# Kernel optimization log

Measured on AMD Instinct MI355X. Metric: run time of the kernel, lower is better.

Reference implementation:

```python
import jax, jax.numpy as jnp
import numpy as np

S = 14        # grid size
B = 2         # boxes per cell
NC = 20       # classes
N = 4096      # batch
L_COORD = 5.0
L_NOOBJ = 0.5


def _xywh2xyxy(b):
    # b[..., :2] are cell-center coords (scaled by 1/S), b[..., 2:4] are w,h
    xy = b[..., :2] / S
    wh = b[..., 2:4]
    return jnp.concatenate([xy - 0.5 * wh, xy + 0.5 * wh], axis=-1)


def _iou(b1, b2):
    # elementwise (broadcasting) IoU over last dim [x1,y1,x2,y2]
    lt = jnp.maximum(b1[..., :2], b2[..., :2])
    rb = jnp.minimum(b1[..., 2:4], b2[..., 2:4])
    wh = jnp.clip(rb - lt, 0.0)
    inter = wh[..., 0] * wh[..., 1]
    a1 = (b1[..., 2] - b1[..., 0]) * (b1[..., 3] - b1[..., 1])
    a2 = (b2[..., 2] - b2[..., 0]) * (b2[..., 3] - b2[..., 1])
    return inter / (a1 + a2 - inter)


def setup_inputs() -> dict:
    key = jax.random.key(0)
    k1, k2, k3, k4 = jax.random.split(key, 4)
    pred_tensor = jax.random.uniform(k1, (N, S, S, B * 5 + NC), dtype=jnp.float32)
    target_boxes = jax.random.uniform(k2, (N, S, S, 4), dtype=jnp.float32)
    target_cls = jax.random.uniform(k3, (N, S, S, NC), dtype=jnp.float32)
    has_object_map = jax.random.bernoulli(k4, 0.15, (N, S, S))
    return dict(pred_tensor=pred_tensor, target_boxes=target_boxes,
                target_cls=target_cls, has_object_map=has_object_map)


def reference(pred_tensor, target_boxes, target_cls, has_object_map):
    n = pred_tensor.shape[0]
    pb = pred_tensor[..., :B * 5].reshape(n, S, S, B, 5)   # (N,S,S,B,5)
    pcls = pred_tensor[..., B * 5:]                        # (N,S,S,20)
    m = has_object_map                                     # (N,S,S) bool
    mf = m.astype(pred_tensor.dtype)

    # class loss: masked sum of squares over object cells
    cls_loss = jnp.sum(jnp.where(m[..., None], (pcls - target_cls) ** 2, 0.0))

    # no-object loss: confidence^2 summed over non-object cells, both boxes
    noobj_loss = jnp.sum(jnp.where(~m[..., None], pb[..., 4] ** 2, 0.0))

    # best-iou box selection (iou is treated as ground truth: no gradient)
    iou = _iou(_xywh2xyxy(pb[..., :4]),
               _xywh2xyxy(target_boxes)[..., None, :])    # (N,S,S,B)
    iou = jax.lax.stop_gradient(iou)
    best = jnp.argmax(iou, axis=-1)                        # (N,S,S)
    best_iou = jnp.max(iou, axis=-1)                       # (N,S,S)
    resp = jnp.take_along_axis(pb, best[..., None, None], axis=3)[..., 0, :]  # (N,S,S,5)

    reg_loss = (jnp.sum(mf[..., None] * (resp[..., :2] - target_boxes[..., :2]) ** 2)
                + jnp.sum(mf[..., None] * (jnp.sqrt(resp[..., 2:4])
                                           - jnp.sqrt(target_boxes[..., 2:4])) ** 2))

    # containing-object confidence loss vs best iou (target detached)
    contain_loss = jnp.sum(mf * (resp[..., 4] - best_iou) ** 2)

    total = (L_COORD * reg_loss + L_NOOBJ * noobj_loss + contain_loss + cls_loss) / n
    return jnp.stack([total, reg_loss, contain_loss, noobj_loss, cls_loss])
```

## Files before the change

### kernel.cpp

```cpp
#include <hip/hip_runtime.h>


#define GS 14
#define NCLS 20
#define BLOCK 256
#define CPT 2
#define CPB (BLOCK * CPT)
#define NSLOTS 64
#define SLOT_STRIDE 16


template <int CB>
__device__ __forceinline__ void cell_compute(const float (&v)[60],
                                             const float4 tb4,
                                             const float* __restrict__ tcls,
                                             int cell, bool m,
                                             float& reg, float& cont,
                                             float& noobj, float& cls) {
    const float invS = 1.0f / (float)GS;
    if (m) {
        const float tx = tb4.x, ty = tb4.y, tw = tb4.z, th = tb4.w;

        const float tcx = tx * invS, tcy = ty * invS;
        const float t_x1 = tcx - 0.5f * tw, t_y1 = tcy - 0.5f * th;
        const float t_x2 = tcx + 0.5f * tw, t_y2 = tcy + 0.5f * th;
        const float ta = (t_x2 - t_x1) * (t_y2 - t_y1);

        const float b0x = v[CB + 0], b0y = v[CB + 1], b0w = v[CB + 2], b0h = v[CB + 3], b0c = v[CB + 4];
        const float b1x = v[CB + 5], b1y = v[CB + 6], b1w = v[CB + 7], b1h = v[CB + 8], b1c = v[CB + 9];

        float iou0, iou1;
        {
            const float cx = b0x * invS, cy = b0y * invS;
            const float x1 = cx - 0.5f * b0w, y1 = cy - 0.5f * b0h;
            const float x2 = cx + 0.5f * b0w, y2 = cy + 0.5f * b0h;
            const float iw = fmaxf(fminf(x2, t_x2) - fmaxf(x1, t_x1), 0.0f);
            const float ih = fmaxf(fminf(y2, t_y2) - fmaxf(y1, t_y1), 0.0f);
            const float inter = iw * ih;
            const float pa = (x2 - x1) * (y2 - y1);
            iou0 = inter / (pa + ta - inter);
        }
        {
            const float cx = b1x * invS, cy = b1y * invS;
            const float x1 = cx - 0.5f * b1w, y1 = cy - 0.5f * b1h;
            const float x2 = cx + 0.5f * b1w, y2 = cy + 0.5f * b1h;
            const float iw = fmaxf(fminf(x2, t_x2) - fmaxf(x1, t_x1), 0.0f);
            const float ih = fmaxf(fminf(y2, t_y2) - fmaxf(y1, t_y1), 0.0f);
            const float inter = iw * ih;
            const float pa = (x2 - x1) * (y2 - y1);
            iou1 = inter / (pa + ta - inter);
        }

        const bool sel1 = iou1 > iou0;
        const float biou = fmaxf(iou0, iou1);
        const float rx = sel1 ? b1x : b0x;
        const float ry = sel1 ? b1y : b0y;
        const float rw = sel1 ? b1w : b0w;
        const float rh = sel1 ? b1h : b0h;
        const float rc = sel1 ? b1c : b0c;

        const float d0 = rx - tx, d1 = ry - ty;
        const float d2 = sqrtf(rw) - sqrtf(tw);
        const float d3 = sqrtf(rh) - sqrtf(th);
        reg += d0 * d0 + d1 * d1 + d2 * d2 + d3 * d3;

        const float dc = rc - biou;
        cont += dc * dc;

        const float4* tc4 = reinterpret_cast<const float4*>(tcls + (size_t)cell * NCLS);
        float csum = 0.0f;
        #pragma unroll
        for (int j = 0; j < 5; ++j) {
            const float4 t4 = tc4[j];
            float d;
            d = v[CB + 10 + j * 4 + 0] - t4.x; csum += d * d;
            d = v[CB + 10 + j * 4 + 1] - t4.y; csum += d * d;
            d = v[CB + 10 + j * 4 + 2] - t4.z; csum += d * d;
            d = v[CB + 10 + j * 4 + 3] - t4.w; csum += d * d;
        }
        cls += csum;
    } else {
        const float c0 = v[CB + 4], c1 = v[CB + 9];
        noobj += c0 * c0 + c1 * c1;
    }
}

__launch_bounds__(BLOCK)
__global__ void yolo_loss_kernel(const float* __restrict__ pred,
                                 const float* __restrict__ tbox,
                                 const float* __restrict__ tcls,
                                 const void* __restrict__ mask,
                                 float* __restrict__ ws,
                                 int ncells) {
    const int tid = threadIdx.x;

    int my_gt1 = 0, my_nzoff = 0;
    if (ncells >= 4096) {
        const uint4 w4 = reinterpret_cast<const uint4*>(mask)[tid];
        const unsigned a = w4.x | w4.y | w4.z | w4.w;
        my_gt1   = (a & 0xFEFEFEFEu) != 0;
        my_nzoff = (a & 0xFFFFFF00u) != 0;
    } else if (tid == 0) {
        const unsigned char* mb = (const unsigned char*)mask;
        for (int i = 0; i < ncells; ++i) {
            if (mb[i] > 1) my_gt1 = 1;
            if ((i & 3) != 0 && mb[i] != 0) my_nzoff = 1;
        }
    }
    const int gt1   = __syncthreads_or(my_gt1);
    const int nzoff = __syncthreads_or(my_nzoff);
    const int fmt = gt1 ? 2 : (nzoff ? 1 : 0);

    const int g = blockIdx.x * BLOCK + tid;
    const int c0 = g * CPT;

    float reg = 0.0f, cont = 0.0f, noobj = 0.0f, cls = 0.0f;

    if (c0 + CPT <= ncells) {
        float v[60];
        float4* v4 = reinterpret_cast<float4*>(v);
        const float4* prow = reinterpret_cast<const float4*>(pred) + (size_t)g * 15;
        #pragma unroll
        for (int j = 0; j < 15; ++j) v4[j] = prow[j];

        bool m0, m1;
        if (fmt == 2) {
            const float2 mm = reinterpret_cast<const float2*>(mask)[g];
            m0 = mm.x != 0.0f; m1 = mm.y != 0.0f;
        } else if (fmt == 1) {
            const uchar2 mm = reinterpret_cast<const uchar2*>(mask)[g];
            m0 = mm.x != 0; m1 = mm.y != 0;
        } else {
            const int2 mm = reinterpret_cast<const int2*>(mask)[g];
            m0 = mm.x != 0; m1 = mm.y != 0;
        }

        const float4 tb0 = reinterpret_cast<const float4*>(tbox)[c0];
        const float4 tb1 = reinterpret_cast<const float4*>(tbox)[c0 + 1];

        cell_compute<0>(v, tb0, tcls, c0,     m0, reg, cont, noobj, cls);
        cell_compute<30>(v, tb1, tcls, c0 + 1, m1, reg, cont, noobj, cls);
    } else if (c0 < ncells) {
        for (int cell = c0; cell < ncells; ++cell) {
            bool m;
            if (fmt == 2)      m = ((const float*)mask)[cell] != 0.0f;
            else if (fmt == 1) m = ((const unsigned char*)mask)[cell] != 0;
            else               m = ((const int*)mask)[cell] != 0;
            float v[60];
            #pragma unroll
            for (int f = 0; f < 30; ++f) v[f] = pred[(size_t)cell * 30 + f];
            float4 tb;
            tb.x = tbox[(size_t)cell * 4 + 0];
            tb.y = tbox[(size_t)cell * 4 + 1];
            tb.z = tbox[(size_t)cell * 4 + 2];
            tb.w = tbox[(size_t)cell * 4 + 3];
            cell_compute<0>(v, tb, tcls, cell, m, reg, cont, noobj, cls);
        }
    }

    #pragma unroll
    for (int off = 32; off > 0; off >>= 1) {
        reg   += __shfl_down(reg, off);
        cont  += __shfl_down(cont, off);
        noobj += __shfl_down(noobj, off);
        cls   += __shfl_down(cls, off);
    }

    __shared__ float sred[4][4];
    const int wave = tid >> 6;
    if ((tid & 63) == 0) {
        sred[wave][0] = reg; sred[wave][1] = cont;
        sred[wave][2] = noobj; sred[wave][3] = cls;
    }
    __syncthreads();
    if (tid == 0) {
        float r = 0, c = 0, no = 0, cl = 0;
        #pragma unroll
        for (int w = 0; w < 4; ++w) {
            r += sred[w][0]; c += sred[w][1]; no += sred[w][2]; cl += sred[w][3];
        }
        float* slot = ws + (size_t)(blockIdx.x & (NSLOTS - 1)) * SLOT_STRIDE;
        atomicAdd(&slot[0], r);
        atomicAdd(&slot[1], c);
        atomicAdd(&slot[2], no);
        atomicAdd(&slot[3], cl);
    }
}

__global__ void yolo_finalize_kernel(const float* __restrict__ ws,
                                     float* __restrict__ out, float inv_n) {
    const int t = threadIdx.x;
    float reg   = ws[t * SLOT_STRIDE + 0];
    float cont  = ws[t * SLOT_STRIDE + 1];
    float noobj = ws[t * SLOT_STRIDE + 2];
    float cls   = ws[t * SLOT_STRIDE + 3];
    #pragma unroll
    for (int off = 32; off > 0; off >>= 1) {
        reg   += __shfl_down(reg, off);
        cont  += __shfl_down(cont, off);
        noobj += __shfl_down(noobj, off);
        cls   += __shfl_down(cls, off);
    }
    if (t == 0) {
        const float total = (5.0f * reg + 0.5f * noobj + cont + cls) * inv_n;
        out[0] = total;
        out[1] = reg;
        out[2] = cont;
        out[3] = noobj;
        out[4] = cls;
    }
}

extern "C" void kernel_launch(void* const* d_in, const int* in_sizes, int n_in,
                              void* d_out, int out_size, void* d_ws, size_t ws_size,
                              hipStream_t stream) {
    const float* pred = (const float*)d_in[0];
    const float* tbox = (const float*)d_in[1];
    const float* tcls = (const float*)d_in[2];
    const void*  mask = d_in[3];
    float* ws  = (float*)d_ws;
    float* out = (float*)d_out;

    const int ncells = in_sizes[3];
    const int n_img  = ncells / (GS * GS);
    const float inv_n = 1.0f / (float)n_img;

    hipMemsetAsync(ws, 0, NSLOTS * SLOT_STRIDE * sizeof(float), stream);

    const int grid = (ncells + CPB - 1) / CPB;
    yolo_loss_kernel<<<grid, BLOCK, 0, stream>>>(pred, tbox, tcls, mask, ws, ncells);

    yolo_finalize_kernel<<<1, 64, 0, stream>>>(ws, out, inv_n);
}
```

Before: 34.95 us.

## Skip unneeded pred loads for empty cell pairs and fuse finalize via last-block reduction

Loads only the float4s holding the confidence values for both cells up front, and fetches the rest of the prediction row only when at least one of the two cells has an object. This cuts HBM traffic for the roughly 72% of pairs with no object. It also removes the separate finalize kernel: each block writes its partials to its own slot, and the last block to arrive (found with an atomic counter) reduces all slots and writes the output. The counter reset is folded into a smaller memset. The cost is a threadfence plus atomic per block, and the last block reduces serially over about 1568 slots.

```diff
diff --git a/kernel.cpp b/kernel.cpp
--- a/kernel.cpp
+++ b/kernel.cpp
@@ -6,9 +6,8 @@
 #define BLOCK 256
 #define CPT 2
 #define CPB (BLOCK * CPT)
-#define NSLOTS 64
-#define SLOT_STRIDE 16
-
+
+#define WS_SLOT0 16
 
 template <int CB>
 __device__ __forceinline__ void cell_compute(const float (&v)[60],
@@ -91,25 +90,25 @@
                                  const float* __restrict__ tcls,
                                  const void* __restrict__ mask,
                                  float* __restrict__ ws,
-                                 int ncells) {
+                                 int ncells, float inv_n,
+                                 float* __restrict__ out) {
     const int tid = threadIdx.x;
 
-    int my_gt1 = 0, my_nzoff = 0;
+    int my_bits = 0;
     if (ncells >= 4096) {
         const uint4 w4 = reinterpret_cast<const uint4*>(mask)[tid];
         const unsigned a = w4.x | w4.y | w4.z | w4.w;
-        my_gt1   = (a & 0xFEFEFEFEu) != 0;
-        my_nzoff = (a & 0xFFFFFF00u) != 0;
+        my_bits  = ((a & 0xFEFEFEFEu) != 0) ? 2 : 0;
+        my_bits |= ((a & 0xFFFFFF00u) != 0) ? 1 : 0;
     } else if (tid == 0) {
         const unsigned char* mb = (const unsigned char*)mask;
         for (int i = 0; i < ncells; ++i) {
-            if (mb[i] > 1) my_gt1 = 1;
-            if ((i & 3) != 0 && mb[i] != 0) my_nzoff = 1;
-        }
-    }
-    const int gt1   = __syncthreads_or(my_gt1);
-    const int nzoff = __syncthreads_or(my_nzoff);
-    const int fmt = gt1 ? 2 : (nzoff ? 1 : 0);
+            if (mb[i] > 1) my_bits |= 2;
+            if ((i & 3) != 0 && mb[i] != 0) my_bits |= 1;
+        }
+    }
+    const int bits = __syncthreads_or(my_bits);
+    const int fmt = (bits & 2) ? 2 : ((bits & 1) ? 1 : 0);
 
     const int g = blockIdx.x * BLOCK + tid;
     const int c0 = g * CPT;
@@ -120,8 +119,11 @@
         float v[60];
         float4* v4 = reinterpret_cast<float4*>(v);
         const float4* prow = reinterpret_cast<const float4*>(pred) + (size_t)g * 15;
-        #pragma unroll
-        for (int j = 0; j < 15; ++j) v4[j] = prow[j];
+
+        v4[1] = prow[1];
+        v4[2] = prow[2];
+        v4[8] = prow[8];
+        v4[9] = prow[9];
 
         bool m0, m1;
         if (fmt == 2) {
@@ -137,6 +139,14 @@
 
         const float4 tb0 = reinterpret_cast<const float4*>(tbox)[c0];
         const float4 tb1 = reinterpret_cast<const float4*>(tbox)[c0 + 1];
+
+        if (m0 | m1) {
+            v4[0] = prow[0];
+            v4[3] = prow[3]; v4[4] = prow[4]; v4[5] = prow[5];
+            v4[6] = prow[6]; v4[7] = prow[7];
+            v4[10] = prow[10]; v4[11] = prow[11]; v4[12] = prow[12];
+            v4[13] = prow[13]; v4[14] = prow[14];
+        }
 
         cell_compute<0>(v, tb0, tcls, c0,     m0, reg, cont, noobj, cls);
         cell_compute<30>(v, tb1, tcls, c0 + 1, m1, reg, cont, noobj, cls);
@@ -167,47 +177,58 @@
     }
 
     __shared__ float sred[4][4];
+    __shared__ int s_last;
     const int wave = tid >> 6;
     if ((tid & 63) == 0) {
         sred[wave][0] = reg; sred[wave][1] = cont;
         sred[wave][2] = noobj; sred[wave][3] = cls;
     }
     __syncthreads();
+
     if (tid == 0) {
         float r = 0, c = 0, no = 0, cl = 0;
         #pragma unroll
         for (int w = 0; w < 4; ++w) {
             r += sred[w][0]; c += sred[w][1]; no += sred[w][2]; cl += sred[w][3];
         }
-        float* slot = ws + (size_t)(blockIdx.x & (NSLOTS - 1)) * SLOT_STRIDE;
-        atomicAdd(&slot[0], r);
-        atomicAdd(&slot[1], c);
-        atomicAdd(&slot[2], no);
-        atomicAdd(&slot[3], cl);
-    }
-}
-
-__global__ void yolo_finalize_kernel(const float* __restrict__ ws,
-                                     float* __restrict__ out, float inv_n) {
-    const int t = threadIdx.x;
-    float reg   = ws[t * SLOT_STRIDE + 0];
-    float cont  = ws[t * SLOT_STRIDE + 1];
-    float noobj = ws[t * SLOT_STRIDE + 2];
-    float cls   = ws[t * SLOT_STRIDE + 3];
-    #pragma unroll
-    for (int off = 32; off > 0; off >>= 1) {
-        reg   += __shfl_down(reg, off);
-        cont  += __shfl_down(cont, off);
-        noobj += __shfl_down(noobj, off);
-        cls   += __shfl_down(cls, off);
-    }
-    if (t == 0) {
-        const float total = (5.0f * reg + 0.5f * noobj + cont + cls) * inv_n;
-        out[0] = total;
-        out[1] = reg;
-        out[2] = cont;
-        out[3] = noobj;
-        out[4] = cls;
+        reinterpret_cast<float4*>(ws + WS_SLOT0)[blockIdx.x] = make_float4(r, c, no, cl);
+        __threadfence();
+        const int prev = atomicAdd((int*)ws, 1);
+        s_last = (prev == (int)gridDim.x - 1);
+    }
+    __syncthreads();
+
+    if (s_last) {
+        __threadfence();
+        float r = 0, c = 0, no = 0, cl = 0;
+        for (int b = tid; b < (int)gridDim.x; b += BLOCK) {
+            const float4 p = reinterpret_cast<const float4*>(ws + WS_SLOT0)[b];
+            r += p.x; c += p.y; no += p.z; cl += p.w;
+        }
+        #pragma unroll
+        for (int off = 32; off > 0; off >>= 1) {
+            r  += __shfl_down(r, off);
+            c  += __shfl_down(c, off);
+            no += __shfl_down(no, off);
+            cl += __shfl_down(cl, off);
+        }
+        if ((tid & 63) == 0) {
+            sred[wave][0] = r; sred[wave][1] = c;
+            sred[wave][2] = no; sred[wave][3] = cl;
+        }
+        __syncthreads();
+        if (tid == 0) {
+            float R = 0, C = 0, NO = 0, CL = 0;
+            #pragma unroll
+            for (int w = 0; w < 4; ++w) {
+                R += sred[w][0]; C += sred[w][1]; NO += sred[w][2]; CL += sred[w][3];
+            }
+            out[0] = (5.0f * R + 0.5f * NO + C + CL) * inv_n;
+            out[1] = R;
+            out[2] = C;
+            out[3] = NO;
+            out[4] = CL;
+        }
     }
 }
 
@@ -225,10 +246,9 @@
     const int n_img  = ncells / (GS * GS);
     const float inv_n = 1.0f / (float)n_img;
 
-    hipMemsetAsync(ws, 0, NSLOTS * SLOT_STRIDE * sizeof(float), stream);
+    hipMemsetAsync(ws, 0, sizeof(int), stream);
 
     const int grid = (ncells + CPB - 1) / CPB;
-    yolo_loss_kernel<<<grid, BLOCK, 0, stream>>>(pred, tbox, tcls, mask, ws, ncells);
-
-    yolo_finalize_kernel<<<1, 64, 0, stream>>>(ws, out, inv_n);
+    yolo_loss_kernel<<<grid, BLOCK, 0, stream>>>(pred, tbox, tcls, mask, ws,
+                                                 ncells, inv_n, out);
 }
```

New measurement: 84.61 us. 2.42x slower.

## Split confidence-sum pass from object-cell pass and skip loads for empty cells

Applied to the files above, without the earlier changes.

The kernel now launches two interleaved block roles. One role streams the whole prediction tensor with coalesced float4 loads and sums the squared confidences of all cells. The other role loads prediction rows, target boxes and class targets only for object cells, then subtracts their confidences from the no-object sum. The goal is to cut the memory traffic of the per-cell pass, where about 85% of cells have no object. The catch is that the prediction tensor is still read in full, only ~2/15 of the float4 lines are useful in the streaming pass, and the subtraction can add floating-point cancellation.

```diff
diff --git a/kernel.cpp b/kernel.cpp
--- a/kernel.cpp
+++ b/kernel.cpp
@@ -12,13 +12,14 @@
 
 template <int CB>
 __device__ __forceinline__ void cell_compute(const float (&v)[60],
-                                             const float4 tb4,
+                                             const float* __restrict__ tbox,
                                              const float* __restrict__ tcls,
                                              int cell, bool m,
                                              float& reg, float& cont,
                                              float& noobj, float& cls) {
     const float invS = 1.0f / (float)GS;
     if (m) {
+        const float4 tb4 = reinterpret_cast<const float4*>(tbox)[cell];
         const float tx = tb4.x, ty = tb4.y, tw = tb4.z, th = tb4.w;
 
         const float tcx = tx * invS, tcy = ty * invS;
@@ -67,6 +68,8 @@
         const float dc = rc - biou;
         cont += dc * dc;
 
+        noobj -= b0c * b0c + b1c * b1c;
+
         const float4* tc4 = reinterpret_cast<const float4*>(tcls + (size_t)cell * NCLS);
         float csum = 0.0f;
         #pragma unroll
@@ -79,50 +82,78 @@
             d = v[CB + 10 + j * 4 + 3] - t4.w; csum += d * d;
         }
         cls += csum;
-    } else {
-        const float c0 = v[CB + 4], c1 = v[CB + 9];
-        noobj += c0 * c0 + c1 * c1;
     }
 }
 
 __launch_bounds__(BLOCK)
-__global__ void yolo_loss_kernel(const float* __restrict__ pred,
+__global__ void yolo_main_kernel(const float* __restrict__ pred,
                                  const float* __restrict__ tbox,
                                  const float* __restrict__ tcls,
                                  const void* __restrict__ mask,
                                  float* __restrict__ ws,
-                                 int ncells) {
+                                 int ncells, int nsub) {
     const int tid = threadIdx.x;
-
-    int my_gt1 = 0, my_nzoff = 0;
+    const int role = blockIdx.x & 1;
+    const int sub = blockIdx.x >> 1;
+
+    if (role == 0) {
+        const float4* p4 = reinterpret_cast<const float4*>(pred);
+        const long long nf4 = ((long long)ncells * 30) >> 2;
+        const long long stride = (long long)nsub * BLOCK;
+        long long idx = (long long)sub * BLOCK + tid;
+        int p = (int)((idx << 2) % 30);
+        const int pstep = (int)((stride << 2) % 30);
+        float s = 0.0f;
+        #pragma unroll 5
+        for (; idx < nf4; idx += stride) {
+            const float4 f = p4[idx];
+            const float val = (p == 4) ? f.x
+                            : (p == 8) ? f.y
+                            : (p == 2) ? f.z
+                            : (p == 6) ? f.w : 0.0f;
+            s += val * val;
+            p += pstep; if (p >= 30) p -= 30;
+        }
+        if (sub == 0 && tid == 0) {
+            for (long long o = nf4 << 2; o < (long long)ncells * 30; ++o) {
+                const int r = (int)(o % 30);
+                if (r == 4 || r == 9) { const float x = pred[o]; s += x * x; }
+            }
+        }
+        #pragma unroll
+        for (int off = 32; off > 0; off >>= 1) s += __shfl_down(s, off);
+        __shared__ float sred1[4];
+        if ((tid & 63) == 0) sred1[tid >> 6] = s;
+        __syncthreads();
+        if (tid == 0) {
+            const float t = sred1[0] + sred1[1] + sred1[2] + sred1[3];
+            atomicAdd(ws + (size_t)(blockIdx.x & (NSLOTS - 1)) * SLOT_STRIDE + 2, t);
+        }
+        return;
+    }
+
+    int my_bits = 0;
     if (ncells >= 4096) {
         const uint4 w4 = reinterpret_cast<const uint4*>(mask)[tid];
         const unsigned a = w4.x | w4.y | w4.z | w4.w;
-        my_gt1   = (a & 0xFEFEFEFEu) != 0;
-        my_nzoff = (a & 0xFFFFFF00u) != 0;
+        my_bits  = ((a & 0xFEFEFEFEu) != 0) ? 2 : 0;
+        my_bits |= ((a & 0xFFFFFF00u) != 0) ? 1 : 0;
     } else if (tid == 0) {
         const unsigned char* mb = (const unsigned char*)mask;
         for (int i = 0; i < ncells; ++i) {
-            if (mb[i] > 1) my_gt1 = 1;
-            if ((i & 3) != 0 && mb[i] != 0) my_nzoff = 1;
-        }
-    }
-    const int gt1   = __syncthreads_or(my_gt1);
-    const int nzoff = __syncthreads_or(my_nzoff);
-    const int fmt = gt1 ? 2 : (nzoff ? 1 : 0);
-
-    const int g = blockIdx.x * BLOCK + tid;
+            if (mb[i] > 1) my_bits |= 2;
+            if ((i & 3) != 0 && mb[i] != 0) my_bits |= 1;
+        }
+    }
+    const int bits = __syncthreads_or(my_bits);
+    const int fmt = (bits & 2) ? 2 : ((bits & 1) ? 1 : 0);
+
+    const int g = sub * BLOCK + tid;
     const int c0 = g * CPT;
 
     float reg = 0.0f, cont = 0.0f, noobj = 0.0f, cls = 0.0f;
 
     if (c0 + CPT <= ncells) {
-        float v[60];
-        float4* v4 = reinterpret_cast<float4*>(v);
-        const float4* prow = reinterpret_cast<const float4*>(pred) + (size_t)g * 15;
-        #pragma unroll
-        for (int j = 0; j < 15; ++j) v4[j] = prow[j];
-
         bool m0, m1;
         if (fmt == 2) {
             const float2 mm = reinterpret_cast<const float2*>(mask)[g];
@@ -135,11 +166,20 @@
             m0 = mm.x != 0; m1 = mm.y != 0;
         }
 
-        const float4 tb0 = reinterpret_cast<const float4*>(tbox)[c0];
-        const float4 tb1 = reinterpret_cast<const float4*>(tbox)[c0 + 1];
-
-        cell_compute<0>(v, tb0, tcls, c0,     m0, reg, cont, noobj, cls);
-        cell_compute<30>(v, tb1, tcls, c0 + 1, m1, reg, cont, noobj, cls);
+        float v[60];
+        float4* v4 = reinterpret_cast<float4*>(v);
+        const float4* prow = reinterpret_cast<const float4*>(pred) + (size_t)g * 15;
+        if (m0) {
+            #pragma unroll
+            for (int j = 0; j < 8; ++j) v4[j] = prow[j];
+        }
+        if (m1) {
+            #pragma unroll
+            for (int j = 7; j < 15; ++j) v4[j] = prow[j];
+        }
+
+        cell_compute<0>(v, tbox, tcls, c0,     m0, reg, cont, noobj, cls);
+        cell_compute<30>(v, tbox, tcls, c0 + 1, m1, reg, cont, noobj, cls);
     } else if (c0 < ncells) {
         for (int cell = c0; cell < ncells; ++cell) {
             bool m;
@@ -147,14 +187,11 @@
             else if (fmt == 1) m = ((const unsigned char*)mask)[cell] != 0;
             else               m = ((const int*)mask)[cell] != 0;
             float v[60];
-            #pragma unroll
-            for (int f = 0; f < 30; ++f) v[f] = pred[(size_t)cell * 30 + f];
-            float4 tb;
-            tb.x = tbox[(size_t)cell * 4 + 0];
-            tb.y = tbox[(size_t)cell * 4 + 1];
-            tb.z = tbox[(size_t)cell * 4 + 2];
-            tb.w = tbox[(size_t)cell * 4 + 3];
-            cell_compute<0>(v, tb, tcls, cell, m, reg, cont, noobj, cls);
+            if (m) {
+                #pragma unroll
+                for (int f = 0; f < 30; ++f) v[f] = pred[(size_t)cell * 30 + f];
+            }
+            cell_compute<0>(v, tbox, tcls, cell, m, reg, cont, noobj, cls);
         }
     }
 
@@ -165,7 +202,6 @@
         noobj += __shfl_down(noobj, off);
         cls   += __shfl_down(cls, off);
     }
-
     __shared__ float sred[4][4];
     const int wave = tid >> 6;
     if ((tid & 63) == 0) {
@@ -227,8 +263,10 @@
 
     hipMemsetAsync(ws, 0, NSLOTS * SLOT_STRIDE * sizeof(float), stream);
 
-    const int grid = (ncells + CPB - 1) / CPB;
-    yolo_loss_kernel<<<grid, BLOCK, 0, stream>>>(pred, tbox, tcls, mask, ws, ncells);
+    const int nblk_obj = (ncells + CPB - 1) / CPB;
+    const int grid = 2 * nblk_obj;
+    yolo_main_kernel<<<grid, BLOCK, 0, stream>>>(pred, tbox, tcls, mask, ws,
+                                                 ncells, nblk_obj);
 
     yolo_finalize_kernel<<<1, 64, 0, stream>>>(ws, out, inv_n);
 }
```

Measured after the change: 50.12 us. 43.4% more time.

## Stage prediction rows through LDS with direct global-to-LDS loads, one cell per thread

Applied to the files above, without the earlier changes.

Each wave now copies its contiguous 64-cell slab of the prediction tensor into shared memory with global_load_lds in coalesced 16-byte chunks, then each thread reads its 30-float row from LDS. This replaces the strided per-thread float4 row loads with fully coalesced accesses. The work split also drops from two cells per thread to one, doubling the grid. The two format-detection reductions are merged into a single __syncthreads_or on a bitmask. It adds LDS usage (30 KB per block) and an explicit vmcnt wait.

```diff
diff --git a/kernel.cpp b/kernel.cpp
--- a/kernel.cpp
+++ b/kernel.cpp
@@ -4,14 +4,24 @@
 #define GS 14
 #define NCLS 20
 #define BLOCK 256
-#define CPT 2
-#define CPB (BLOCK * CPT)
 #define NSLOTS 64
 #define SLOT_STRIDE 16
-
-
-template <int CB>
-__device__ __forceinline__ void cell_compute(const float (&v)[60],
+#define WAVE_F 1920
+#define SLAB_F (4 * WAVE_F)
+
+
+__device__ __forceinline__ void gload_lds16(const float* g, float* l) {
+    __builtin_amdgcn_global_load_lds(
+        (const __attribute__((address_space(1))) void*)g,
+        (__attribute__((address_space(3))) void*)l, 16, 0, 0);
+}
+__device__ __forceinline__ void gload_lds4(const float* g, float* l) {
+    __builtin_amdgcn_global_load_lds(
+        (const __attribute__((address_space(1))) void*)g,
+        (__attribute__((address_space(3))) void*)l, 4, 0, 0);
+}
+
+__device__ __forceinline__ void cell_compute(const float (&v)[30],
                                              const float4 tb4,
                                              const float* __restrict__ tcls,
                                              int cell, bool m,
@@ -26,8 +36,8 @@
         const float t_x2 = tcx + 0.5f * tw, t_y2 = tcy + 0.5f * th;
         const float ta = (t_x2 - t_x1) * (t_y2 - t_y1);
 
-        const float b0x = v[CB + 0], b0y = v[CB + 1], b0w = v[CB + 2], b0h = v[CB + 3], b0c = v[CB + 4];
-        const float b1x = v[CB + 5], b1y = v[CB + 6], b1w = v[CB + 7], b1h = v[CB + 8], b1c = v[CB + 9];
+        const float b0x = v[0], b0y = v[1], b0w = v[2], b0h = v[3], b0c = v[4];
+        const float b1x = v[5], b1y = v[6], b1w = v[7], b1h = v[8], b1c = v[9];
 
         float iou0, iou1;
         {
@@ -73,14 +83,14 @@
         for (int j = 0; j < 5; ++j) {
             const float4 t4 = tc4[j];
             float d;
-            d = v[CB + 10 + j * 4 + 0] - t4.x; csum += d * d;
-            d = v[CB + 10 + j * 4 + 1] - t4.y; csum += d * d;
-            d = v[CB + 10 + j * 4 + 2] - t4.z; csum += d * d;
-            d = v[CB + 10 + j * 4 + 3] - t4.w; csum += d * d;
+            d = v[10 + j * 4 + 0] - t4.x; csum += d * d;
+            d = v[10 + j * 4 + 1] - t4.y; csum += d * d;
+            d = v[10 + j * 4 + 2] - t4.z; csum += d * d;
+            d = v[10 + j * 4 + 3] - t4.w; csum += d * d;
         }
         cls += csum;
     } else {
-        const float c0 = v[CB + 4], c1 = v[CB + 9];
+        const float c0 = v[4], c1 = v[9];
         noobj += c0 * c0 + c1 * c1;
     }
 }
@@ -92,70 +102,75 @@
                                  const void* __restrict__ mask,
                                  float* __restrict__ ws,
                                  int ncells) {
+    __shared__ float slab[SLAB_F];
     const int tid = threadIdx.x;
-
-    int my_gt1 = 0, my_nzoff = 0;
+    const int wv = tid >> 6;
+    const int lane = tid & 63;
+
+    int my_bits = 0;
     if (ncells >= 4096) {
         const uint4 w4 = reinterpret_cast<const uint4*>(mask)[tid];
         const unsigned a = w4.x | w4.y | w4.z | w4.w;
-        my_gt1   = (a & 0xFEFEFEFEu) != 0;
-        my_nzoff = (a & 0xFFFFFF00u) != 0;
+        my_bits  = ((a & 0xFEFEFEFEu) != 0) ? 2 : 0;
+        my_bits |= ((a & 0xFFFFFF00u) != 0) ? 1 : 0;
     } else if (tid == 0) {
         const unsigned char* mb = (const unsigned char*)mask;
         for (int i = 0; i < ncells; ++i) {
-            if (mb[i] > 1) my_gt1 = 1;
-            if ((i & 3) != 0 && mb[i] != 0) my_nzoff = 1;
-        }
-    }
-    const int gt1   = __syncthreads_or(my_gt1);
-    const int nzoff = __syncthreads_or(my_nzoff);
-    const int fmt = gt1 ? 2 : (nzoff ? 1 : 0);
-
-    const int g = blockIdx.x * BLOCK + tid;
-    const int c0 = g * CPT;
+            if (mb[i] > 1) my_bits |= 2;
+            if ((i & 3) != 0 && mb[i] != 0) my_bits |= 1;
+        }
+    }
+    const int bits = __syncthreads_or(my_bits);
+    const int fmt = (bits & 2) ? 2 : ((bits & 1) ? 1 : 0);
+
+    const int base = blockIdx.x * BLOCK;
+    const int cell = base + tid;
 
     float reg = 0.0f, cont = 0.0f, noobj = 0.0f, cls = 0.0f;
 
-    if (c0 + CPT <= ncells) {
-        float v[60];
-        float4* v4 = reinterpret_cast<float4*>(v);
-        const float4* prow = reinterpret_cast<const float4*>(pred) + (size_t)g * 15;
-        #pragma unroll
-        for (int j = 0; j < 15; ++j) v4[j] = prow[j];
-
-        bool m0, m1;
-        if (fmt == 2) {
-            const float2 mm = reinterpret_cast<const float2*>(mask)[g];
-            m0 = mm.x != 0.0f; m1 = mm.y != 0.0f;
-        } else if (fmt == 1) {
-            const uchar2 mm = reinterpret_cast<const uchar2*>(mask)[g];
-            m0 = mm.x != 0; m1 = mm.y != 0;
-        } else {
-            const int2 mm = reinterpret_cast<const int2*>(mask)[g];
-            m0 = mm.x != 0; m1 = mm.y != 0;
-        }
-
-        const float4 tb0 = reinterpret_cast<const float4*>(tbox)[c0];
-        const float4 tb1 = reinterpret_cast<const float4*>(tbox)[c0 + 1];
-
-        cell_compute<0>(v, tb0, tcls, c0,     m0, reg, cont, noobj, cls);
-        cell_compute<30>(v, tb1, tcls, c0 + 1, m1, reg, cont, noobj, cls);
-    } else if (c0 < ncells) {
-        for (int cell = c0; cell < ncells; ++cell) {
-            bool m;
-            if (fmt == 2)      m = ((const float*)mask)[cell] != 0.0f;
-            else if (fmt == 1) m = ((const unsigned char*)mask)[cell] != 0;
-            else               m = ((const int*)mask)[cell] != 0;
-            float v[60];
-            #pragma unroll
-            for (int f = 0; f < 30; ++f) v[f] = pred[(size_t)cell * 30 + f];
-            float4 tb;
-            tb.x = tbox[(size_t)cell * 4 + 0];
-            tb.y = tbox[(size_t)cell * 4 + 1];
-            tb.z = tbox[(size_t)cell * 4 + 2];
-            tb.w = tbox[(size_t)cell * 4 + 3];
-            cell_compute<0>(v, tb, tcls, cell, m, reg, cont, noobj, cls);
-        }
+    if (base + BLOCK <= ncells) {
+        const float* gsrc = pred + (size_t)blockIdx.x * SLAB_F + wv * WAVE_F;
+        float* ldst = slab + wv * WAVE_F;
+        #pragma unroll
+        for (int i = 0; i < 7; ++i)
+            gload_lds16(gsrc + i * 256 + lane * 4, ldst + i * 256);
+        #pragma unroll
+        for (int k = 0; k < 2; ++k)
+            gload_lds4(gsrc + 1792 + k * 64 + lane, ldst + 1792 + k * 64);
+
+        bool m;
+        if (fmt == 2)      m = ((const float*)mask)[cell] != 0.0f;
+        else if (fmt == 1) m = ((const unsigned char*)mask)[cell] != 0;
+        else               m = ((const int*)mask)[cell] != 0;
+        const float4 tb4 = reinterpret_cast<const float4*>(tbox)[cell];
+
+        asm volatile("s_waitcnt vmcnt(0)" ::: "memory");
+        __builtin_amdgcn_sched_barrier(0);
+
+        float v[30];
+        const float* lrow = slab + wv * WAVE_F + lane * 30;
+        #pragma unroll
+        for (int j = 0; j < 7; ++j)
+            *reinterpret_cast<float4*>(&v[j * 4]) =
+                *reinterpret_cast<const float4*>(lrow + j * 4);
+        *reinterpret_cast<float2*>(&v[28]) =
+            *reinterpret_cast<const float2*>(lrow + 28);
+
+        cell_compute(v, tb4, tcls, cell, m, reg, cont, noobj, cls);
+    } else if (cell < ncells) {
+        bool m;
+        if (fmt == 2)      m = ((const float*)mask)[cell] != 0.0f;
+        else if (fmt == 1) m = ((const unsigned char*)mask)[cell] != 0;
+        else               m = ((const int*)mask)[cell] != 0;
+        float v[30];
+        #pragma unroll
+        for (int f = 0; f < 30; ++f) v[f] = pred[(size_t)cell * 30 + f];
+        float4 tb;
+        tb.x = tbox[(size_t)cell * 4 + 0];
+        tb.y = tbox[(size_t)cell * 4 + 1];
+        tb.z = tbox[(size_t)cell * 4 + 2];
+        tb.w = tbox[(size_t)cell * 4 + 3];
+        cell_compute(v, tb, tcls, cell, m, reg, cont, noobj, cls);
     }
 
     #pragma unroll
@@ -167,10 +182,9 @@
     }
 
     __shared__ float sred[4][4];
-    const int wave = tid >> 6;
-    if ((tid & 63) == 0) {
-        sred[wave][0] = reg; sred[wave][1] = cont;
-        sred[wave][2] = noobj; sred[wave][3] = cls;
+    if (lane == 0) {
+        sred[wv][0] = reg; sred[wv][1] = cont;
+        sred[wv][2] = noobj; sred[wv][3] = cls;
     }
     __syncthreads();
     if (tid == 0) {
@@ -227,7 +241,7 @@
 
     hipMemsetAsync(ws, 0, NSLOTS * SLOT_STRIDE * sizeof(float), stream);
 
-    const int grid = (ncells + CPB - 1) / CPB;
+    const int grid = (ncells + BLOCK - 1) / BLOCK;
     yolo_loss_kernel<<<grid, BLOCK, 0, stream>>>(pred, tbox, tcls, mask, ws, ncells);
 
     yolo_finalize_kernel<<<1, 64, 0, stream>>>(ws, out, inv_n);
```

Measured after the change: 33.47 us. 4.2% less time.
